# Performance work log

Hardware: AMD Instinct MI355X
Metric: run time of the kernel (lower is better)

The kernel has to match this reference:

```python
import jax, jax.numpy as jnp
import numpy as np

B, T, N, D = 16, 1024, 1024, 256   # batch, query len (hp.max_T), key len (hp.max_N), hp.d
WIN = 64                            # hp.attention_win_size
NEG = jnp.float32(-2**32 + 1)       # padding value used by the TF module


def setup_inputs() -> dict:
    key = jax.random.key(0)
    k1, k2, k3, k4 = jax.random.split(key, 4)
    Q = jax.random.normal(k1, (B, T, D), dtype=jnp.float32)
    K = jax.random.normal(k2, (B, N, D), dtype=jnp.float32)
    V = jax.random.normal(k3, (B, N, D), dtype=jnp.float32)
    prev_max_attentions = jax.random.randint(k4, (B,), 0, N - WIN, dtype=jnp.int64)
    return {"Q": Q, "K": K, "V": V, "prev_max_attentions": prev_max_attentions}


def reference(Q, K, V, prev_max_attentions):
    # scaled scores: [B, T, N]
    A = jnp.einsum("btd,bnd->btn", Q, K) * jax.lax.rsqrt(jnp.float32(D))

    # monotonic window mask (mono_attention=True):
    idx = jnp.arange(N)                              # [N]
    prev = prev_max_attentions[:, None]              # [B, 1]
    masks = (idx < prev) | (idx >= prev + WIN)       # [B, N], True = disallowed
    A = jnp.where(masks[:, None, :], NEG, A)         # broadcast over T (== tf.tile)

    A = jax.nn.softmax(A, axis=-1)                   # [B, T, N]
    max_attentions = jnp.argmax(A, axis=-1).astype(jnp.float32)  # [B, T]

    R = jnp.concatenate([jnp.einsum("btn,bnd->btd", A, V), Q], axis=-1)  # [B, T, 2D]
    alignments = jnp.transpose(A, (0, 2, 1))         # [B, N, T]
    return (R, alignments, max_attentions)
```

## Files before the change

### kernel.cpp

```cpp
#include <hip/hip_runtime.h>


#define BB 16
#define TT 1024
#define NN 1024
#define DD 256
#define WIN 64

#define R_ELEMS   (16u*1024u*512u)
#define ALN_ELEMS (16u*1024u*1024u)

__global__ __launch_bounds__(64) void attn_kernel(
    const float* __restrict__ Q, const float* __restrict__ K,
    const float* __restrict__ V, const int* __restrict__ prev_in,
    float* __restrict__ out)
{
    float* Rout   = out;
    float* aligns = out + R_ELEMS;
    float* maxatt = out + R_ELEMS + ALN_ELEMS;

    const int lane  = threadIdx.x;
    const int group = blockIdx.x;
    const int b  = group >> 8;
    const int t0 = (group & 255) * 4;
    const int prev = prev_in[b];

    const float* qb = Q + ((size_t)b * TT + t0) * DD;
    const float4* K4 = (const float4*)(K + ((size_t)b * NN + prev + lane) * DD);

    float acc[4] = {0.f, 0.f, 0.f, 0.f};
    for (int d4 = 0; d4 < DD / 4; ++d4) {
        float4 k = K4[d4];
        #pragma unroll
        for (int t = 0; t < 4; ++t) {
            float4 q = ((const float4*)(qb + t * DD))[d4];
            acc[t] += q.x * k.x + q.y * k.y + q.z * k.z + q.w * k.w;
        }
    }

    float p[4];
    #pragma unroll
    for (int t = 0; t < 4; ++t) {
        float v = acc[t] * 0.0625f;

        float m = v;
        #pragma unroll
        for (int off = 32; off; off >>= 1)
            m = fmaxf(m, __shfl_xor(m, off));

        float e = expf(v - m);
        float s = e;
        #pragma unroll
        for (int off = 32; off; off >>= 1)
            s += __shfl_xor(s, off);

        p[t] = e / s;

        float av = v; int ai = lane;
        #pragma unroll
        for (int off = 32; off; off >>= 1) {
            float ov = __shfl_xor(av, off);
            int   oi = __shfl_xor(ai, off);
            if (ov > av || (ov == av && oi < ai)) { av = ov; ai = oi; }
        }
        if (lane == 0)
            maxatt[(size_t)b * TT + t0 + t] = (float)(prev + ai);

        aligns[(size_t)b * NN * TT + (size_t)(prev + lane) * TT + (t0 + t)] = p[t];
    }

    const float4* V4 = (const float4*)(V + ((size_t)b * NN + prev) * DD);
    float4 o[4];
    #pragma unroll
    for (int t = 0; t < 4; ++t) o[t] = make_float4(0.f, 0.f, 0.f, 0.f);

    for (int j = 0; j < WIN; ++j) {
        float4 vv = V4[(size_t)j * (DD / 4) + lane];
        #pragma unroll
        for (int t = 0; t < 4; ++t) {
            float pj = __shfl(p[t], j);
            o[t].x += pj * vv.x;
            o[t].y += pj * vv.y;
            o[t].z += pj * vv.z;
            o[t].w += pj * vv.w;
        }
    }

    #pragma unroll
    for (int t = 0; t < 4; ++t) {
        float* Rrow = Rout + ((size_t)b * TT + t0 + t) * (2 * DD);
        ((float4*)Rrow)[lane] = o[t];
        ((float4*)(Rrow + DD))[lane] = ((const float4*)(qb + t * DD))[lane];
    }
}

extern "C" void kernel_launch(void* const* d_in, const int* in_sizes, int n_in,
                              void* d_out, int out_size, void* d_ws, size_t ws_size,
                              hipStream_t stream) {
    const float* Q = (const float*)d_in[0];
    const float* K = (const float*)d_in[1];
    const float* V = (const float*)d_in[2];
    const int* prev = (const int*)d_in[3];
    float* out = (float*)d_out;

    hipMemsetAsync(out + R_ELEMS, 0, (size_t)ALN_ELEMS * sizeof(float), stream);

    attn_kernel<<<BB * TT / 4, 64, 0, stream>>>(Q, K, V, prev, out);
}
```

Measured before the change: 191.1 us.

## Fuse alignment zero-fill into kernel with 16-query blocks and shared-memory staging

```diff
diff --git a/kernel.cpp b/kernel.cpp
--- a/kernel.cpp
+++ b/kernel.cpp
@@ -6,26 +6,31 @@
 #define NN 1024
 #define DD 256
 #define WIN 64
+#define TBLK 16
 
 #define R_ELEMS   (16u*1024u*512u)
 #define ALN_ELEMS (16u*1024u*1024u)
 
-__global__ __launch_bounds__(64) void attn_kernel(
+__global__ __launch_bounds__(256) void attn_kernel(
     const float* __restrict__ Q, const float* __restrict__ K,
     const float* __restrict__ V, const int* __restrict__ prev_in,
     float* __restrict__ out)
 {
+    __shared__ float p_a[WIN][TBLK + 1];
+    __shared__ float p_t[TBLK][WIN + 4];
+
     float* Rout   = out;
     float* aligns = out + R_ELEMS;
     float* maxatt = out + R_ELEMS + ALN_ELEMS;
 
-    const int lane  = threadIdx.x;
-    const int group = blockIdx.x;
-    const int b  = group >> 8;
-    const int t0 = (group & 255) * 4;
+    const int tid  = threadIdx.x;
+    const int lane = tid & 63;
+    const int w    = tid >> 6;
+    const int b    = blockIdx.x >> 6;
+    const int t0   = (blockIdx.x & 63) * TBLK;
     const int prev = prev_in[b];
 
-    const float* qb = Q + ((size_t)b * TT + t0) * DD;
+    const float*  qb = Q + ((size_t)b * TT + t0 + w * 4) * DD;
     const float4* K4 = (const float4*)(K + ((size_t)b * NN + prev + lane) * DD);
 
     float acc[4] = {0.f, 0.f, 0.f, 0.f};
@@ -34,27 +39,27 @@
         #pragma unroll
         for (int t = 0; t < 4; ++t) {
             float4 q = ((const float4*)(qb + t * DD))[d4];
-            acc[t] += q.x * k.x + q.y * k.y + q.z * k.z + q.w * k.w;
+            acc[t] = fmaf(q.x, k.x, fmaf(q.y, k.y, fmaf(q.z, k.z, fmaf(q.w, k.w, acc[t]))));
         }
     }
 
-    float p[4];
     #pragma unroll
     for (int t = 0; t < 4; ++t) {
         float v = acc[t] * 0.0625f;
 
         float m = v;
         #pragma unroll
-        for (int off = 32; off; off >>= 1)
-            m = fmaxf(m, __shfl_xor(m, off));
+        for (int off = 32; off; off >>= 1) m = fmaxf(m, __shfl_xor(m, off));
 
         float e = expf(v - m);
         float s = e;
         #pragma unroll
-        for (int off = 32; off; off >>= 1)
-            s += __shfl_xor(s, off);
+        for (int off = 32; off; off >>= 1) s += __shfl_xor(s, off);
 
-        p[t] = e / s;
+        float p = e / s;
+        const int tt = w * 4 + t;
+        p_a[lane][tt] = p;
+        p_t[tt][lane] = p;
 
         float av = v; int ai = lane;
         #pragma unroll
@@ -63,34 +68,55 @@
             int   oi = __shfl_xor(ai, off);
             if (ov > av || (ov == av && oi < ai)) { av = ov; ai = oi; }
         }
-        if (lane == 0)
-            maxatt[(size_t)b * TT + t0 + t] = (float)(prev + ai);
+        if (lane == 0) maxatt[(size_t)b * TT + t0 + tt] = (float)(prev + ai);
+    }
+    __syncthreads();
 
-        aligns[(size_t)b * NN * TT + (size_t)(prev + lane) * TT + (t0 + t)] = p[t];
-    }
-
-    const float4* V4 = (const float4*)(V + ((size_t)b * NN + prev) * DD);
-    float4 o[4];
-    #pragma unroll
-    for (int t = 0; t < 4; ++t) o[t] = make_float4(0.f, 0.f, 0.f, 0.f);
-
-    for (int j = 0; j < WIN; ++j) {
-        float4 vv = V4[(size_t)j * (DD / 4) + lane];
+    {
+        const int rsub = tid >> 2;
+        const int cg   = tid & 3;
+        float* abase = aligns + (size_t)b * NN * TT + t0 + cg * 4;
         #pragma unroll
-        for (int t = 0; t < 4; ++t) {
-            float pj = __shfl(p[t], j);
-            o[t].x += pj * vv.x;
-            o[t].y += pj * vv.y;
-            o[t].z += pj * vv.z;
-            o[t].w += pj * vv.w;
+        for (int it = 0; it < NN / 64; ++it) {
+            int n  = it * 64 + rsub;
+            int iw = n - prev;
+            float4 val = make_float4(0.f, 0.f, 0.f, 0.f);
+            if ((unsigned)iw < WIN) {
+                val.x = p_a[iw][cg * 4 + 0];
+                val.y = p_a[iw][cg * 4 + 1];
+                val.z = p_a[iw][cg * 4 + 2];
+                val.w = p_a[iw][cg * 4 + 3];
+            }
+            *(float4*)(abase + (size_t)n * TT) = val;
         }
     }
 
-    #pragma unroll
-    for (int t = 0; t < 4; ++t) {
-        float* Rrow = Rout + ((size_t)b * TT + t0 + t) * (2 * DD);
-        ((float4*)Rrow)[lane] = o[t];
-        ((float4*)(Rrow + DD))[lane] = ((const float4*)(qb + t * DD))[lane];
+    {
+        const int tl = tid >> 4;
+        const int dc0 = tid & 15;
+        const float4* V4 = (const float4*)(V + ((size_t)b * NN + prev) * DD);
+        const float4* Q4 = (const float4*)(Q + ((size_t)b * TT + t0 + tl) * DD);
+        float4* R4 = (float4*)(Rout + ((size_t)b * TT + t0 + tl) * (2 * DD));
+
+        #pragma unroll
+        for (int pass = 0; pass < 4; ++pass) {
+            const int dc = pass * 16 + dc0;
+            float4 o = make_float4(0.f, 0.f, 0.f, 0.f);
+            #pragma unroll 4
+            for (int j4 = 0; j4 < WIN / 4; ++j4) {
+                float4 p4 = *(const float4*)&p_t[tl][j4 * 4];
+                float4 v0 = V4[(size_t)(j4 * 4 + 0) * (DD / 4) + dc];
+                float4 v1 = V4[(size_t)(j4 * 4 + 1) * (DD / 4) + dc];
+                float4 v2 = V4[(size_t)(j4 * 4 + 2) * (DD / 4) + dc];
+                float4 v3 = V4[(size_t)(j4 * 4 + 3) * (DD / 4) + dc];
+                o.x = fmaf(p4.x, v0.x, fmaf(p4.y, v1.x, fmaf(p4.z, v2.x, fmaf(p4.w, v3.x, o.x))));
+                o.y = fmaf(p4.x, v0.y, fmaf(p4.y, v1.y, fmaf(p4.z, v2.y, fmaf(p4.w, v3.y, o.y))));
+                o.z = fmaf(p4.x, v0.z, fmaf(p4.y, v1.z, fmaf(p4.z, v2.z, fmaf(p4.w, v3.z, o.z))));
+                o.w = fmaf(p4.x, v0.w, fmaf(p4.y, v1.w, fmaf(p4.z, v2.w, fmaf(p4.w, v3.w, o.w))));
+            }
+            R4[dc] = o;
+            R4[DD / 4 + dc] = Q4[dc];
+        }
     }
 }
 
@@ -103,7 +129,5 @@
     const int* prev = (const int*)d_in[3];
     float* out = (float*)d_out;
 
-    hipMemsetAsync(out + R_ELEMS, 0, (size_t)ALN_ELEMS * sizeof(float), stream);
-
-    attn_kernel<<<BB * TT / 4, 64, 0, stream>>>(Q, K, V, prev, out);
+    attn_kernel<<<BB * TT / TBLK, 256, 0, stream>>>(Q, K, V, prev, out);
 }
```

After: 227.8 us. +19.2%, slower.

## Fuse alignment zero-fill into kernel and stage K window in shared memory

Applied to the files above, without the earlier changes.

```diff
diff --git a/kernel.cpp b/kernel.cpp
--- a/kernel.cpp
+++ b/kernel.cpp
@@ -6,55 +6,72 @@
 #define NN 1024
 #define DD 256
 #define WIN 64
+#define TBLK 32
+#define NTHREADS 512
 
 #define R_ELEMS   (16u*1024u*512u)
 #define ALN_ELEMS (16u*1024u*1024u)
 
-__global__ __launch_bounds__(64) void attn_kernel(
+#define KS_STRIDE 260
+
+__global__ __launch_bounds__(NTHREADS, 4) void attn_v4(
     const float* __restrict__ Q, const float* __restrict__ K,
     const float* __restrict__ V, const int* __restrict__ prev_in,
     float* __restrict__ out)
 {
+    __shared__ float ks[WIN * KS_STRIDE];
+    __shared__ float p_lds[TBLK][WIN + 4];
+
     float* Rout   = out;
     float* aligns = out + R_ELEMS;
     float* maxatt = out + R_ELEMS + ALN_ELEMS;
 
-    const int lane  = threadIdx.x;
-    const int group = blockIdx.x;
-    const int b  = group >> 8;
-    const int t0 = (group & 255) * 4;
+    const int tid  = threadIdx.x;
+    const int lane = tid & 63;
+    const int w    = tid >> 6;
+    const int b    = blockIdx.x >> 5;
+    const int t0   = (blockIdx.x & 31) * TBLK;
     const int prev = prev_in[b];
 
-    const float* qb = Q + ((size_t)b * TT + t0) * DD;
-    const float4* K4 = (const float4*)(K + ((size_t)b * NN + prev + lane) * DD);
+    {
+        const float4* Ksrc = (const float4*)(K + ((size_t)b * NN + prev) * DD);
+        #pragma unroll
+        for (int k = 0; k < 8; ++k) {
+            int t4 = tid + k * NTHREADS;
+            int r  = t4 >> 6;
+            int c  = t4 & 63;
+            float4 v = Ksrc[t4];
+            *(float4*)&ks[r * KS_STRIDE + c * 4] = v;
+        }
+    }
+    __syncthreads();
 
+    const float* qb = Q + ((size_t)b * TT + t0 + w * 4) * DD;
     float acc[4] = {0.f, 0.f, 0.f, 0.f};
+    #pragma unroll 4
     for (int d4 = 0; d4 < DD / 4; ++d4) {
-        float4 k = K4[d4];
+        float4 kk = *(const float4*)&ks[lane * KS_STRIDE + d4 * 4];
         #pragma unroll
         for (int t = 0; t < 4; ++t) {
             float4 q = ((const float4*)(qb + t * DD))[d4];
-            acc[t] += q.x * k.x + q.y * k.y + q.z * k.z + q.w * k.w;
+            acc[t] = fmaf(q.x, kk.x, fmaf(q.y, kk.y, fmaf(q.z, kk.z, fmaf(q.w, kk.w, acc[t]))));
         }
     }
 
-    float p[4];
     #pragma unroll
     for (int t = 0; t < 4; ++t) {
         float v = acc[t] * 0.0625f;
 
         float m = v;
         #pragma unroll
-        for (int off = 32; off; off >>= 1)
-            m = fmaxf(m, __shfl_xor(m, off));
+        for (int off = 32; off; off >>= 1) m = fmaxf(m, __shfl_xor(m, off));
 
         float e = expf(v - m);
         float s = e;
         #pragma unroll
-        for (int off = 32; off; off >>= 1)
-            s += __shfl_xor(s, off);
+        for (int off = 32; off; off >>= 1) s += __shfl_xor(s, off);
 
-        p[t] = e / s;
+        p_lds[w * 4 + t][lane] = e / s;
 
         float av = v; int ai = lane;
         #pragma unroll
@@ -63,34 +80,58 @@
             int   oi = __shfl_xor(ai, off);
             if (ov > av || (ov == av && oi < ai)) { av = ov; ai = oi; }
         }
-        if (lane == 0)
-            maxatt[(size_t)b * TT + t0 + t] = (float)(prev + ai);
-
-        aligns[(size_t)b * NN * TT + (size_t)(prev + lane) * TT + (t0 + t)] = p[t];
+        if (lane == 0) maxatt[(size_t)b * TT + t0 + w * 4 + t] = (float)(prev + ai);
     }
 
-    const float4* V4 = (const float4*)(V + ((size_t)b * NN + prev) * DD);
-    float4 o[4];
-    #pragma unroll
-    for (int t = 0; t < 4; ++t) o[t] = make_float4(0.f, 0.f, 0.f, 0.f);
+    {
+        const float4* V4 = (const float4*)(V + ((size_t)b * NN + prev) * DD);
+        float4 o[4];
+        #pragma unroll
+        for (int t = 0; t < 4; ++t) o[t] = make_float4(0.f, 0.f, 0.f, 0.f);
 
-    for (int j = 0; j < WIN; ++j) {
-        float4 vv = V4[(size_t)j * (DD / 4) + lane];
+        #pragma unroll 2
+        for (int j4 = 0; j4 < WIN / 4; ++j4) {
+            float4 vv0 = V4[(size_t)(j4 * 4 + 0) * (DD / 4) + lane];
+            float4 vv1 = V4[(size_t)(j4 * 4 + 1) * (DD / 4) + lane];
+            float4 vv2 = V4[(size_t)(j4 * 4 + 2) * (DD / 4) + lane];
+            float4 vv3 = V4[(size_t)(j4 * 4 + 3) * (DD / 4) + lane];
+            #pragma unroll
+            for (int t = 0; t < 4; ++t) {
+                float4 p4 = *(const float4*)&p_lds[w * 4 + t][j4 * 4];
+                o[t].x = fmaf(p4.x, vv0.x, fmaf(p4.y, vv1.x, fmaf(p4.z, vv2.x, fmaf(p4.w, vv3.x, o[t].x))));
+                o[t].y = fmaf(p4.x, vv0.y, fmaf(p4.y, vv1.y, fmaf(p4.z, vv2.y, fmaf(p4.w, vv3.y, o[t].y))));
+                o[t].z = fmaf(p4.x, vv0.z, fmaf(p4.y, vv1.z, fmaf(p4.z, vv2.z, fmaf(p4.w, vv3.z, o[t].z))));
+                o[t].w = fmaf(p4.x, vv0.w, fmaf(p4.y, vv1.w, fmaf(p4.z, vv2.w, fmaf(p4.w, vv3.w, o[t].w))));
+            }
+        }
+
         #pragma unroll
         for (int t = 0; t < 4; ++t) {
-            float pj = __shfl(p[t], j);
-            o[t].x += pj * vv.x;
-            o[t].y += pj * vv.y;
-            o[t].z += pj * vv.z;
-            o[t].w += pj * vv.w;
+            float* Rrow = Rout + ((size_t)b * TT + t0 + w * 4 + t) * (2 * DD);
+            ((float4*)Rrow)[lane] = o[t];
+            float4 qv = ((const float4*)(qb + t * DD))[lane];
+            ((float4*)(Rrow + DD))[lane] = qv;
         }
     }
+    __syncthreads();
 
-    #pragma unroll
-    for (int t = 0; t < 4; ++t) {
-        float* Rrow = Rout + ((size_t)b * TT + t0 + t) * (2 * DD);
-        ((float4*)Rrow)[lane] = o[t];
-        ((float4*)(Rrow + DD))[lane] = ((const float4*)(qb + t * DD))[lane];
+    {
+        const int rgrp = tid >> 3;
+        const int cg   = tid & 7;
+        float* abase = aligns + (size_t)b * NN * TT + t0 + cg * 4;
+        #pragma unroll 4
+        for (int pass = 0; pass < 16; ++pass) {
+            int row = pass * 64 + rgrp;
+            int iw  = row - prev;
+            float4 v = make_float4(0.f, 0.f, 0.f, 0.f);
+            if ((unsigned)iw < WIN) {
+                v.x = p_lds[cg * 4 + 0][iw];
+                v.y = p_lds[cg * 4 + 1][iw];
+                v.z = p_lds[cg * 4 + 2][iw];
+                v.w = p_lds[cg * 4 + 3][iw];
+            }
+            *(float4*)(abase + (size_t)row * TT) = v;
+        }
     }
 }
 
@@ -103,7 +144,5 @@
     const int* prev = (const int*)d_in[3];
     float* out = (float*)d_out;
 
-    hipMemsetAsync(out + R_ELEMS, 0, (size_t)ALN_ELEMS * sizeof(float), stream);
-
-    attn_kernel<<<BB * TT / 4, 64, 0, stream>>>(Q, K, V, prev, out);
+    attn_v4<<<BB * TT / TBLK, NTHREADS, 0, stream>>>(Q, K, V, prev, out);
 }
```

Measured after the change: 178.2 us. 1.07x faster.

## Stage K/V windows in LDS across 16 queries per block with coalesced alignment stores

Applied to the files above, without the earlier changes.

```diff
diff --git a/kernel.cpp b/kernel.cpp
--- a/kernel.cpp
+++ b/kernel.cpp
@@ -6,55 +6,81 @@
 #define NN 1024
 #define DD 256
 #define WIN 64
+#define TBLK 16
+#define NT 512
 
 #define R_ELEMS   (16u*1024u*512u)
 #define ALN_ELEMS (16u*1024u*1024u)
 
-__global__ __launch_bounds__(64) void attn_kernel(
+#define LSTR 132
+
+__global__ __launch_bounds__(256) void zero_aligns(float4* __restrict__ p) {
+    const float4 z = make_float4(0.f, 0.f, 0.f, 0.f);
+    size_t base = (size_t)blockIdx.x * 1024 + threadIdx.x;
+    #pragma unroll
+    for (int k = 0; k < 4; ++k) p[base + k * 256] = z;
+}
+
+__global__ __launch_bounds__(NT, 8) void attn_v5(
     const float* __restrict__ Q, const float* __restrict__ K,
     const float* __restrict__ V, const int* __restrict__ prev_in,
     float* __restrict__ out)
 {
+    __shared__ float ks[WIN * LSTR];
+    __shared__ float p_lds[TBLK][WIN + 4];
+
     float* Rout   = out;
     float* aligns = out + R_ELEMS;
     float* maxatt = out + R_ELEMS + ALN_ELEMS;
 
-    const int lane  = threadIdx.x;
-    const int group = blockIdx.x;
-    const int b  = group >> 8;
-    const int t0 = (group & 255) * 4;
+    const int tid  = threadIdx.x;
+    const int lane = tid & 63;
+    const int w    = tid >> 6;
+    const int b    = blockIdx.x >> 6;
+    const int t0   = (blockIdx.x & 63) * TBLK;
     const int prev = prev_in[b];
 
-    const float* qb = Q + ((size_t)b * TT + t0) * DD;
-    const float4* K4 = (const float4*)(K + ((size_t)b * NN + prev + lane) * DD);
+    const float* qb = Q + ((size_t)b * TT + t0 + 2 * w) * DD;
 
-    float acc[4] = {0.f, 0.f, 0.f, 0.f};
-    for (int d4 = 0; d4 < DD / 4; ++d4) {
-        float4 k = K4[d4];
+    float acc0 = 0.f, acc1 = 0.f;
+    #pragma unroll
+    for (int h = 0; h < 2; ++h) {
+        if (h) __syncthreads();
+        const float4* Ksrc = (const float4*)(K + ((size_t)b * NN + prev) * DD + h * 128);
         #pragma unroll
-        for (int t = 0; t < 4; ++t) {
-            float4 q = ((const float4*)(qb + t * DD))[d4];
-            acc[t] += q.x * k.x + q.y * k.y + q.z * k.z + q.w * k.w;
+        for (int k = 0; k < 4; ++k) {
+            int t4 = tid + k * NT;
+            int r = t4 >> 5, c = t4 & 31;
+            float4 v = Ksrc[(size_t)r * 64 + c];
+            *(float4*)&ks[r * LSTR + c * 4] = v;
+        }
+        __syncthreads();
+
+        const float* qh = qb + h * 128;
+        #pragma unroll 8
+        for (int d4 = 0; d4 < 32; ++d4) {
+            float4 kk = *(const float4*)&ks[lane * LSTR + d4 * 4];
+            float4 q0 = ((const float4*)qh)[d4];
+            float4 q1 = ((const float4*)(qh + DD))[d4];
+            acc0 = fmaf(q0.x, kk.x, fmaf(q0.y, kk.y, fmaf(q0.z, kk.z, fmaf(q0.w, kk.w, acc0))));
+            acc1 = fmaf(q1.x, kk.x, fmaf(q1.y, kk.y, fmaf(q1.z, kk.z, fmaf(q1.w, kk.w, acc1))));
         }
     }
 
-    float p[4];
     #pragma unroll
-    for (int t = 0; t < 4; ++t) {
-        float v = acc[t] * 0.0625f;
+    for (int t = 0; t < 2; ++t) {
+        float v = (t ? acc1 : acc0) * 0.0625f;
 
         float m = v;
         #pragma unroll
-        for (int off = 32; off; off >>= 1)
-            m = fmaxf(m, __shfl_xor(m, off));
+        for (int off = 32; off; off >>= 1) m = fmaxf(m, __shfl_xor(m, off));
 
         float e = expf(v - m);
         float s = e;
         #pragma unroll
-        for (int off = 32; off; off >>= 1)
-            s += __shfl_xor(s, off);
+        for (int off = 32; off; off >>= 1) s += __shfl_xor(s, off);
 
-        p[t] = e / s;
+        p_lds[2 * w + t][lane] = e / s;
 
         float av = v; int ai = lane;
         #pragma unroll
@@ -63,34 +89,61 @@
             int   oi = __shfl_xor(ai, off);
             if (ov > av || (ov == av && oi < ai)) { av = ov; ai = oi; }
         }
-        if (lane == 0)
-            maxatt[(size_t)b * TT + t0 + t] = (float)(prev + ai);
-
-        aligns[(size_t)b * NN * TT + (size_t)(prev + lane) * TT + (t0 + t)] = p[t];
+        if (lane == 0) maxatt[(size_t)b * TT + t0 + 2 * w + t] = (float)(prev + ai);
     }
 
-    const float4* V4 = (const float4*)(V + ((size_t)b * NN + prev) * DD);
-    float4 o[4];
+    const int jpar = lane >> 5, dc = lane & 31;
+    float* Rrow = Rout + ((size_t)b * TT + t0 + 2 * w + jpar) * (2 * DD);
+    const int tq0 = 2 * w, tq1 = 2 * w + 1;
+
     #pragma unroll
-    for (int t = 0; t < 4; ++t) o[t] = make_float4(0.f, 0.f, 0.f, 0.f);
+    for (int h = 0; h < 2; ++h) {
+        __syncthreads();
+        const float4* Vsrc = (const float4*)(V + ((size_t)b * NN + prev) * DD + h * 128);
+        #pragma unroll
+        for (int k = 0; k < 4; ++k) {
+            int t4 = tid + k * NT;
+            int r = t4 >> 5, c = t4 & 31;
+            float4 v = Vsrc[(size_t)r * 64 + c];
+            *(float4*)&ks[r * LSTR + c * 4] = v;
+        }
+        __syncthreads();
 
-    for (int j = 0; j < WIN; ++j) {
-        float4 vv = V4[(size_t)j * (DD / 4) + lane];
-        #pragma unroll
-        for (int t = 0; t < 4; ++t) {
-            float pj = __shfl(p[t], j);
-            o[t].x += pj * vv.x;
-            o[t].y += pj * vv.y;
-            o[t].z += pj * vv.z;
-            o[t].w += pj * vv.w;
+        float4 o0 = make_float4(0.f, 0.f, 0.f, 0.f);
+        float4 o1 = make_float4(0.f, 0.f, 0.f, 0.f);
+        #pragma unroll 8
+        for (int j2 = 0; j2 < 32; ++j2) {
+            int j = j2 * 2 + jpar;
+            float4 vv = *(const float4*)&ks[j * LSTR + dc * 4];
+            float pa = p_lds[tq0][j];
+            float pb = p_lds[tq1][j];
+            o0.x = fmaf(pa, vv.x, o0.x); o0.y = fmaf(pa, vv.y, o0.y);
+            o0.z = fmaf(pa, vv.z, o0.z); o0.w = fmaf(pa, vv.w, o0.w);
+            o1.x = fmaf(pb, vv.x, o1.x); o1.y = fmaf(pb, vv.y, o1.y);
+            o1.z = fmaf(pb, vv.z, o1.z); o1.w = fmaf(pb, vv.w, o1.w);
         }
+        o0.x += __shfl_xor(o0.x, 32); o0.y += __shfl_xor(o0.y, 32);
+        o0.z += __shfl_xor(o0.z, 32); o0.w += __shfl_xor(o0.w, 32);
+        o1.x += __shfl_xor(o1.x, 32); o1.y += __shfl_xor(o1.y, 32);
+        o1.z += __shfl_xor(o1.z, 32); o1.w += __shfl_xor(o1.w, 32);
+        float4 ov = jpar ? o1 : o0;
+        ((float4*)Rrow)[h * 32 + dc] = ov;
     }
 
-    #pragma unroll
-    for (int t = 0; t < 4; ++t) {
-        float* Rrow = Rout + ((size_t)b * TT + t0 + t) * (2 * DD);
-        ((float4*)Rrow)[lane] = o[t];
-        ((float4*)(Rrow + DD))[lane] = ((const float4*)(qb + t * DD))[lane];
+    {
+        const float4* Qr = (const float4*)(qb + jpar * DD);
+        ((float4*)(Rrow + DD))[dc]      = Qr[dc];
+        ((float4*)(Rrow + DD))[32 + dc] = Qr[32 + dc];
+    }
+
+    if (tid < 256) {
+        int j = tid >> 2, cg = tid & 3;
+        float4 v;
+        v.x = p_lds[cg * 4 + 0][j];
+        v.y = p_lds[cg * 4 + 1][j];
+        v.z = p_lds[cg * 4 + 2][j];
+        v.w = p_lds[cg * 4 + 3][j];
+        *(float4*)(aligns + ((size_t)b * NN + prev + j) * TT + t0 + cg * 4) = v;
     }
 }
 
@@ -103,7 +156,6 @@
     const int* prev = (const int*)d_in[3];
     float* out = (float*)d_out;
 
-    hipMemsetAsync(out + R_ELEMS, 0, (size_t)ALN_ELEMS * sizeof(float), stream);
-
-    attn_kernel<<<BB * TT / 4, 64, 0, stream>>>(Q, K, V, prev, out);
+    zero_aligns<<<ALN_ELEMS / (4 * 1024), 256, 0, stream>>>((float4*)(out + R_ELEMS));
+    attn_v5<<<BB * TT / TBLK, NT, 0, stream>>>(Q, K, V, prev, out);
 }
```

New measurement: 197.5 us. +3.4%, slower.
